# Kernel optimization log

Measured on AMD Instinct MI355X. Metric: run time of the kernel, lower is better.

## Reference

```python
import jax, jax.numpy as jnp
import numpy as np

B, T, NU, NX = 64, 512, 256, 1024


def setup_inputs() -> dict:
    key = jax.random.key(0)
    ks = jax.random.split(key, 10)
    s = 1.0 / NX  # default uniform_(-1/units, 1/units) init
    w = lambda k, shape: jax.random.uniform(k, shape, jnp.float32, -s, s)
    return {
        "u": jax.random.normal(ks[0], (B, T, NU), jnp.float32),
        "x0": 0.5 * jax.random.normal(ks[1], (B, NX), jnp.float32),
        "Wz": w(ks[2], (NU, NX)), "Uz": w(ks[3], (NX, NX)), "bz": jnp.zeros((NX,), jnp.float32),
        "Wf": w(ks[4], (NU, NX)), "Uf": w(ks[5], (NX, NX)), "bf": jnp.zeros((NX,), jnp.float32),
        "Wr": w(ks[6], (NU, NX)), "Ur": w(ks[7], (NX, NX)), "br": jnp.zeros((NX,), jnp.float32),
    }


def reference(u, x0, Wz, Uz, bz, Wf, Uf, bf, Wr, Ur, br):
    # Precompute input projections for all timesteps (same math, hoisted out of the scan).
    az = jnp.einsum("btu,un->btn", u, Wz) + bz  # (B,T,NX)
    af = jnp.einsum("btu,un->btn", u, Wf) + bf
    ar = jnp.einsum("btu,un->btn", u, Wr) + br
    # time-major for scan
    az, af, ar = (jnp.transpose(a, (1, 0, 2)) for a in (az, af, ar))

    def step(x, inp):
        iz, if_, ir = inp
        z = jax.nn.sigmoid(iz + x @ Uz)            # update gate
        f = jax.nn.sigmoid(if_ + x @ Uf)           # forget gate
        r = jnp.tanh(ir + (f * x) @ Ur)            # squashed candidate
        x_next = z * x + (1.0 - z) * r
        # io_delay=True: output is the state x(k) at the current instant
        return x_next, x

    _, ys = jax.lax.scan(step, x0, (az, af, ar))   # ys: (T,B,NX)
    return jnp.transpose(ys, (1, 0, 2))            # (B,T,NX)
```

## Files before the change

### kernel.cpp

```cpp
#include <hip/hip_runtime.h>
#include <stdint.h>

#define Bsz  64
#define Tsz  512
#define NUsz 256
#define NXsz 1024

#define NGRP 8
#define GWG  32
#define MB   8
#define NC   32

#define SPIN_MAX (1u << 18)

typedef __attribute__((ext_vector_type(8))) short  short8;
typedef __attribute__((ext_vector_type(4))) float  float4v;
typedef unsigned long long ull;

#define FLAGX_OFF   0
#define FLAGFX_OFF  2048
#define XBUF_OFF    4096
#define XBUF_PG     32768
#define FXBUF_OFF   (XBUF_OFF + NGRP * XBUF_PG)

__device__ __forceinline__ short f2bf(float f) {
  unsigned x = __float_as_uint(f);
  return (short)((x + 0x7fffu + ((x >> 16) & 1u)) >> 16);
}

__global__ void gru_init(const float* __restrict__ x0, unsigned char* __restrict__ ws) {
  unsigned idx = blockIdx.x * 256u + threadIdx.x;
  if (idx < 256u)      ((unsigned*)(ws + FLAGX_OFF))[idx] = 1u;
  else if (idx < 512u) ((unsigned*)(ws + FLAGFX_OFF))[idx - 256u] = 0u;
  unsigned g = idx >> 13, c = (idx >> 8) & 31u, b = (idx >> 5) & 7u, cc = idx & 31u;
  float v = x0[(g * MB + b) * NXsz + c * 32u + cc];
  *(short*)(ws + XBUF_OFF + g * XBUF_PG + c * 512u + b * 64u + cc * 2u) = f2bf(v);
}

__device__ __forceinline__ void wait_flags(const unsigned* f, int lane, unsigned need,
                                           unsigned* dead) {
  if (*dead) return;
  const unsigned* p = f + (lane & 31);
  unsigned spins = 0;
  while (true) {
    unsigned v = __hip_atomic_load(p, __ATOMIC_RELAXED, __HIP_MEMORY_SCOPE_AGENT);
    if (__all((int)(v >= need))) break;
    if (++spins > SPIN_MAX) { *dead = 1u; break; }
    __builtin_amdgcn_s_sleep(1);
  }
  __builtin_amdgcn_fence(__ATOMIC_ACQUIRE, "workgroup");
}

__device__ __forceinline__ short8 ldfragB(const float* __restrict__ U, int col, int k0) {
  short8 s;
  #pragma unroll
  for (int e = 0; e < 8; ++e) s[e] = f2bf(U[(long)(k0 + e) * NXsz + col]);
  return s;
}

#define MFMA(a, b, c) __builtin_amdgcn_mfma_f32_16x16x32_bf16((a), (b), (c), 0, 0, 0)

__launch_bounds__(256, 1)
__global__ void gru_persist(const float* __restrict__ u,  const float* __restrict__ x0,
                            const float* __restrict__ Wz, const float* __restrict__ Uz, const float* __restrict__ bz,
                            const float* __restrict__ Wf, const float* __restrict__ Uf, const float* __restrict__ bfp,
                            const float* __restrict__ Wr, const float* __restrict__ Ur, const float* __restrict__ br,
                            float* __restrict__ out, unsigned char* __restrict__ ws)
{
  __shared__ short zfU[2][32][1000];
  __shared__ float part[4][2][8][33];
  __shared__ float xs[8][33];
  __shared__ float bz_s[32], bf_s[32], br_s[32];

  const int bx   = blockIdx.x;
  const int g    = bx & 7;
  const int rank = bx >> 3;
  const int col0 = rank * NC;
  const int tid  = threadIdx.x;
  const int wv   = tid >> 6;
  const int lane = tid & 63;
  const int q    = lane >> 4;
  const int cl   = lane & 15;

  for (int idx = tid; idx < 2 * 32 * 992; idx += 256) {
    int gate = (idx >= 32 * 992);
    int rem  = idx - gate * (32 * 992);
    int k = rem >> 5, n = rem & 31;
    const float* U = gate ? Uf : Uz;
    zfU[gate][n][k] = f2bf(U[(long)k * NXsz + col0 + n]);
  }
  { int b = tid >> 5, n = tid & 31;
    xs[b][n] = x0[(g * MB + b) * NXsz + col0 + n]; }
  if (tid < 32) {
    bz_s[tid] = bz[col0 + tid];
    bf_s[tid] = bfp[col0 + tid];
    br_s[tid] = br[col0 + tid];
  }

  const int bc0 = col0 + cl;
  short8 rU[16], rW[4], zW[4], fW[4], zU31[2], fU31[2];
  #pragma unroll
  for (int i = 0; i < 8; ++i) {
    int k0 = (wv * 8 + i) * 32 + q * 8;
    rU[i*2+0] = ldfragB(Ur, bc0,      k0);
    rU[i*2+1] = ldfragB(Ur, bc0 + 16, k0);
  }
  #pragma unroll
  for (int i = 0; i < 2; ++i) {
    int k0 = (wv * 2 + i) * 32 + q * 8;
    rW[i*2+0] = ldfragB(Wr, bc0, k0);  rW[i*2+1] = ldfragB(Wr, bc0+16, k0);
    zW[i*2+0] = ldfragB(Wz, bc0, k0);  zW[i*2+1] = ldfragB(Wz, bc0+16, k0);
    fW[i*2+0] = ldfragB(Wf, bc0, k0);  fW[i*2+1] = ldfragB(Wf, bc0+16, k0);
  }
  if (wv == 3) {
    zU31[0] = ldfragB(Uz, bc0, 992 + q*8);  zU31[1] = ldfragB(Uz, bc0+16, 992 + q*8);
    fU31[0] = ldfragB(Uf, bc0, 992 + q*8);  fU31[1] = ldfragB(Uf, bc0+16, 992 + q*8);
  } else {
    #pragma unroll
    for (int e = 0; e < 8; ++e) { zU31[0][e]=0; zU31[1][e]=0; fU31[0][e]=0; fU31[1][e]=0; }
  }
  __syncthreads();

  unsigned* flagx  = (unsigned*)(ws + FLAGX_OFF)  + g * GWG;
  unsigned* flagfx = (unsigned*)(ws + FLAGFX_OFF) + g * GWG;
  unsigned char* xb_base  = ws + XBUF_OFF  + (unsigned)g * XBUF_PG;
  unsigned char* fxb_base = ws + FXBUF_OFF + (unsigned)g * XBUF_PG;

  const int b8 = cl & 7;
  const unsigned arow = (unsigned)(b8 * 64 + q * 16);
  const float* u_row = u + (long)(g * MB + b8) * (Tsz * (long)NUsz);

  const int cb  = lane >> 3;
  const int cc0 = (lane & 7) * 4;

  float zreg[4] = {0.f, 0.f, 0.f, 0.f};
  unsigned dead = 0;

  for (int t = 0; t < Tsz; ++t) {
    const unsigned char* xb  = xb_base  + (t & 1) * 16384;
    unsigned char*       fxb = fxb_base + (t & 1) * 16384;

    if (wv == 2) {
      float4v o = { xs[cb][cc0], xs[cb][cc0+1], xs[cb][cc0+2], xs[cb][cc0+3] };
      *(float4v*)(out + (long)(g*MB+cb) * (Tsz*(long)NXsz) + (long)t*NXsz + col0 + cc0) = o;
    }

    short8 au[2];
    #pragma unroll
    for (int i = 0; i < 2; ++i) {
      const float* up = u_row + (long)t * NUsz + (wv*2 + i) * 32 + q * 8;
      float4v a0 = *(const float4v*)up;
      float4v a1 = *(const float4v*)(up + 4);
      short8 s;
      s[0]=f2bf(a0[0]); s[1]=f2bf(a0[1]); s[2]=f2bf(a0[2]); s[3]=f2bf(a0[3]);
      s[4]=f2bf(a1[0]); s[5]=f2bf(a1[1]); s[6]=f2bf(a1[2]); s[7]=f2bf(a1[3]);
      au[i] = s;
    }
    float4v az0 = {0,0,0,0}, az1 = {0,0,0,0}, af0 = {0,0,0,0}, af1 = {0,0,0,0};
    #pragma unroll
    for (int i = 0; i < 2; ++i) {
      az0 = MFMA(au[i], zW[i*2+0], az0);
      az1 = MFMA(au[i], zW[i*2+1], az1);
      af0 = MFMA(au[i], fW[i*2+0], af0);
      af1 = MFMA(au[i], fW[i*2+1], af1);
    }

    wait_flags(flagx, lane, (unsigned)(t + 1), &dead);
    {
      ull ax[16];
      #pragma unroll
      for (int i = 0; i < 8; ++i) {
        const ull* pp = (const ull*)(xb + arow + (unsigned)((wv*8 + i) * 512));
        ax[2*i]   = __hip_atomic_load(pp,     __ATOMIC_RELAXED, __HIP_MEMORY_SCOPE_AGENT);
        ax[2*i+1] = __hip_atomic_load(pp + 1, __ATOMIC_RELAXED, __HIP_MEMORY_SCOPE_AGENT);
      }
      #pragma unroll
      for (int i = 0; i < 8; ++i) {
        union { ull u2[2]; short8 s8; } cv;
        cv.u2[0] = ax[2*i]; cv.u2[1] = ax[2*i+1];
        const int c = wv*8 + i;
        int koff;
        short8 b00, b01, b10, b11;
        if (i == 7) {
          koff = ((wv == 3) ? 0 : c*32) + q*8;
          b00 = *(const short8*)&zfU[0][cl][koff];
          b01 = *(const short8*)&zfU[0][cl+16][koff];
          b10 = *(const short8*)&zfU[1][cl][koff];
          b11 = *(const short8*)&zfU[1][cl+16][koff];
          if (wv == 3) { b00 = zU31[0]; b01 = zU31[1]; b10 = fU31[0]; b11 = fU31[1]; }
        } else {
          koff = c*32 + q*8;
          b00 = *(const short8*)&zfU[0][cl][koff];
          b01 = *(const short8*)&zfU[0][cl+16][koff];
          b10 = *(const short8*)&zfU[1][cl][koff];
          b11 = *(const short8*)&zfU[1][cl+16][koff];
        }
        az0 = MFMA(cv.s8, b00, az0);
        az1 = MFMA(cv.s8, b01, az1);
        af0 = MFMA(cv.s8, b10, af0);
        af1 = MFMA(cv.s8, b11, af1);
      }
    }

    if (q < 2) {
      #pragma unroll
      for (int r = 0; r < 4; ++r) {
        part[wv][0][q*4+r][cl]      = az0[r];
        part[wv][0][q*4+r][cl + 16] = az1[r];
        part[wv][1][q*4+r][cl]      = af0[r];
        part[wv][1][q*4+r][cl + 16] = af1[r];
      }
    }
    __syncthreads();

    if (wv == 0) {
      #pragma unroll
      for (int j = 0; j < 4; ++j) {
        int c = cc0 + j;
        float s = part[0][0][cb][c] + part[1][0][cb][c] + part[2][0][cb][c] + part[3][0][cb][c] + bz_s[c];
        zreg[j] = 1.f / (1.f + __expf(-s));
      }
    } else if (wv == 1) {
      ull pack = 0;
      #pragma unroll
      for (int j = 0; j < 4; ++j) {
        int c = cc0 + j;
        float s = part[0][1][cb][c] + part[1][1][cb][c] + part[2][1][cb][c] + part[3][1][cb][c] + bf_s[c];
        float f = 1.f / (1.f + __expf(-s));
        pack |= (ull)(unsigned short)f2bf(f * xs[cb][c]) << (16 * j);
      }
      __hip_atomic_store((ull*)(fxb + (unsigned)(rank * 512 + lane * 8)), pack,
                         __ATOMIC_RELAXED, __HIP_MEMORY_SCOPE_AGENT);
      __builtin_amdgcn_fence(__ATOMIC_RELEASE, "workgroup");
      if (lane == 0)
        __hip_atomic_store(flagfx + rank, (unsigned)(t + 1),
                           __ATOMIC_RELAXED, __HIP_MEMORY_SCOPE_AGENT);
    }
    __syncthreads();

    float4v ar0 = {0,0,0,0}, ar1 = {0,0,0,0};
    #pragma unroll
    for (int i = 0; i < 2; ++i) {
      ar0 = MFMA(au[i], rW[i*2+0], ar0);
      ar1 = MFMA(au[i], rW[i*2+1], ar1);
    }

    wait_flags(flagfx, lane, (unsigned)(t + 1), &dead);
    {
      ull ax[16];
      #pragma unroll
      for (int i = 0; i < 8; ++i) {
        const ull* pp = (const ull*)(fxb + arow + (unsigned)((wv*8 + i) * 512));
        ax[2*i]   = __hip_atomic_load(pp,     __ATOMIC_RELAXED, __HIP_MEMORY_SCOPE_AGENT);
        ax[2*i+1] = __hip_atomic_load(pp + 1, __ATOMIC_RELAXED, __HIP_MEMORY_SCOPE_AGENT);
      }
      #pragma unroll
      for (int i = 0; i < 8; ++i) {
        union { ull u2[2]; short8 s8; } cv;
        cv.u2[0] = ax[2*i]; cv.u2[1] = ax[2*i+1];
        ar0 = MFMA(cv.s8, rU[i*2+0], ar0);
        ar1 = MFMA(cv.s8, rU[i*2+1], ar1);
      }
    }

    if (q < 2) {
      #pragma unroll
      for (int r = 0; r < 4; ++r) {
        part[wv][0][q*4+r][cl]      = ar0[r];
        part[wv][0][q*4+r][cl + 16] = ar1[r];
      }
    }
    __syncthreads();

    if (wv == 0) {
      unsigned char* xbn = xb_base + ((t + 1) & 1) * 16384;
      ull pack = 0;
      float xnv[4];
      #pragma unroll
      for (int j = 0; j < 4; ++j) {
        int c = cc0 + j;
        float s = part[0][0][cb][c] + part[1][0][cb][c] + part[2][0][cb][c] + part[3][0][cb][c] + br_s[c];
        s = fminf(fmaxf(s, -15.f), 15.f);
        float e  = __expf(2.f * s);
        float rr = (e - 1.f) / (e + 1.f);
        float xn = zreg[j] * xs[cb][c] + (1.f - zreg[j]) * rr;
        xnv[j] = xn;
        pack |= (ull)(unsigned short)f2bf(xn) << (16 * j);
      }
      #pragma unroll
      for (int j = 0; j < 4; ++j) xs[cb][cc0 + j] = xnv[j];
      __hip_atomic_store((ull*)(xbn + (unsigned)(rank * 512 + lane * 8)), pack,
                         __ATOMIC_RELAXED, __HIP_MEMORY_SCOPE_AGENT);
      __builtin_amdgcn_fence(__ATOMIC_RELEASE, "workgroup");
      if (lane == 0)
        __hip_atomic_store(flagx + rank, (unsigned)(t + 2),
                           __ATOMIC_RELAXED, __HIP_MEMORY_SCOPE_AGENT);
    }
    __syncthreads();
  }
}

extern "C" void kernel_launch(void* const* d_in, const int* in_sizes, int n_in,
                              void* d_out, int out_size, void* d_ws, size_t ws_size,
                              hipStream_t stream) {
  (void)in_sizes; (void)n_in; (void)out_size; (void)ws_size;
  const float* u   = (const float*)d_in[0];
  const float* x0  = (const float*)d_in[1];
  const float* Wz  = (const float*)d_in[2];
  const float* Uz  = (const float*)d_in[3];
  const float* bz  = (const float*)d_in[4];
  const float* Wf  = (const float*)d_in[5];
  const float* Uf  = (const float*)d_in[6];
  const float* bfp = (const float*)d_in[7];
  const float* Wr  = (const float*)d_in[8];
  const float* Ur  = (const float*)d_in[9];
  const float* br  = (const float*)d_in[10];
  float* out = (float*)d_out;
  unsigned char* ws = (unsigned char*)d_ws;

  hipLaunchKernelGGL(gru_init, dim3(256), dim3(256), 0, stream, x0, ws);

  void* args[] = { (void*)&u, (void*)&x0, (void*)&Wz, (void*)&Uz, (void*)&bz,
                   (void*)&Wf, (void*)&Uf, (void*)&bfp,
                   (void*)&Wr, (void*)&Ur, (void*)&br, (void*)&out, (void*)&ws };
  hipError_t e = hipLaunchCooperativeKernel((const void*)gru_persist, dim3(256), dim3(256),
                                            args, 0, stream);
  if (e != hipSuccess) {
    hipLaunchKernelGGL(gru_persist, dim3(256), dim3(256), 0, stream,
                       u, x0, Wz, Uz, bz, Wf, Uf, bfp, Wr, Ur, br, out, ws);
  }
}
```

Measured before the change: 3.169 ms.

## Halve persistent grid to 4 groups of 16 batch rows with XCD-aware mapping

Restructures the persistent GRU so each workgroup handles 16 batch rows instead of 8, which uses all 16 MFMA rows rather than discarding half. The grid shrinks to 128 workgroups in 4 groups of 32 column slices, and each group is mapped onto one pair of XCDs so its flag and state traffic stays more local. The exchange buffer layout, publish offsets and init kernel are reworked for the 16-row tiles. This trades half the CU count and more per-workgroup epilogue work for fewer wasted MFMA rows and fewer groups synchronising through memory.

```diff
diff --git a/kernel.cpp b/kernel.cpp
--- a/kernel.cpp
+++ b/kernel.cpp
@@ -6,9 +6,9 @@
 #define NUsz 256
 #define NXsz 1024
 
-#define NGRP 8
+#define NGRP 4
 #define GWG  32
-#define MB   8
+#define MB   16
 #define NC   32
 
 #define SPIN_MAX (1u << 18)
@@ -20,7 +20,7 @@
 #define FLAGX_OFF   0
 #define FLAGFX_OFF  2048
 #define XBUF_OFF    4096
-#define XBUF_PG     32768
+#define XBUF_PG     65536
 #define FXBUF_OFF   (XBUF_OFF + NGRP * XBUF_PG)
 
 __device__ __forceinline__ short f2bf(float f) {
@@ -30,11 +30,14 @@
 
 __global__ void gru_init(const float* __restrict__ x0, unsigned char* __restrict__ ws) {
   unsigned idx = blockIdx.x * 256u + threadIdx.x;
-  if (idx < 256u)      ((unsigned*)(ws + FLAGX_OFF))[idx] = 1u;
-  else if (idx < 512u) ((unsigned*)(ws + FLAGFX_OFF))[idx - 256u] = 0u;
-  unsigned g = idx >> 13, c = (idx >> 8) & 31u, b = (idx >> 5) & 7u, cc = idx & 31u;
-  float v = x0[(g * MB + b) * NXsz + c * 32u + cc];
-  *(short*)(ws + XBUF_OFF + g * XBUF_PG + c * 512u + b * 64u + cc * 2u) = f2bf(v);
+  unsigned* flagx  = (unsigned*)(ws + FLAGX_OFF);
+  unsigned* flagfx = (unsigned*)(ws + FLAGFX_OFF);
+  if (idx < 128u)                       flagx[idx] = 1u;
+  else if (idx >= 256u && idx < 384u)   flagfx[idx - 256u] = 0u;
+  unsigned g = idx >> 14, rem = idx & 16383u;
+  unsigned jj = rem >> 8, b = (rem >> 4) & 15u, k = rem & 15u;
+  float v = x0[(g * 16u + b) * NXsz + jj * 16u + k];
+  *(short*)(ws + XBUF_OFF + g * XBUF_PG + jj * 512u + b * 32u + k * 2u) = f2bf(v);
 }
 
 __device__ __forceinline__ void wait_flags(const unsigned* f, int lane, unsigned need,
@@ -68,19 +71,20 @@
                             float* __restrict__ out, unsigned char* __restrict__ ws)
 {
   __shared__ short zfU[2][32][1000];
-  __shared__ float part[4][2][8][33];
-  __shared__ float xs[8][33];
+  __shared__ float part[4][2][16][33];
+  __shared__ float xs[16][33];
   __shared__ float bz_s[32], bf_s[32], br_s[32];
 
   const int bx   = blockIdx.x;
-  const int g    = bx & 7;
-  const int rank = bx >> 3;
-  const int col0 = rank * NC;
+  const int xcd  = bx & 7;
+  const int g    = xcd >> 1;
+  const int j    = ((xcd & 1) << 4) | (bx >> 3);
   const int tid  = threadIdx.x;
   const int wv   = tid >> 6;
   const int lane = tid & 63;
   const int q    = lane >> 4;
   const int cl   = lane & 15;
+  const int col0 = j * NC;
 
   for (int idx = tid; idx < 2 * 32 * 992; idx += 256) {
     int gate = (idx >= 32 * 992);
@@ -89,8 +93,10 @@
     const float* U = gate ? Uf : Uz;
     zfU[gate][n][k] = f2bf(U[(long)k * NXsz + col0 + n]);
   }
-  { int b = tid >> 5, n = tid & 31;
-    xs[b][n] = x0[(g * MB + b) * NXsz + col0 + n]; }
+  for (int idx = tid; idx < 512; idx += 256) {
+    int b = idx >> 5, n = idx & 31;
+    xs[b][n] = x0[(g * MB + b) * NXsz + col0 + n];
+  }
   if (tid < 32) {
     bz_s[tid] = bz[col0 + tid];
     bf_s[tid] = bfp[col0 + tid];
@@ -123,37 +129,45 @@
 
   unsigned* flagx  = (unsigned*)(ws + FLAGX_OFF)  + g * GWG;
   unsigned* flagfx = (unsigned*)(ws + FLAGFX_OFF) + g * GWG;
-  unsigned char* xb_base  = ws + XBUF_OFF  + (unsigned)g * XBUF_PG;
-  unsigned char* fxb_base = ws + FXBUF_OFF + (unsigned)g * XBUF_PG;
-
-  const int b8 = cl & 7;
-  const unsigned arow = (unsigned)(b8 * 64 + q * 16);
-  const float* u_row = u + (long)(g * MB + b8) * (Tsz * (long)NUsz);
-
-  const int cb  = lane >> 3;
-  const int cc0 = (lane & 7) * 4;
-
-  float zreg[4] = {0.f, 0.f, 0.f, 0.f};
+  unsigned char* xb_base  = ws + XBUF_OFF  + g * XBUF_PG;
+  unsigned char* fxb_base = ws + FXBUF_OFF + g * XBUF_PG;
+
+  const unsigned lane_off = (unsigned)(cl * 32 + (q & 1) * 16 + (q >> 1) * 512);
+
+  const int cb  = lane >> 2;
+  const int cc0 = (lane & 3) << 3;
+  const unsigned pub_off = (unsigned)((2*j + (cc0 >> 4)) * 512 + cb * 32 + (cc0 & 15) * 2);
+
+  const long uTN = (long)Tsz * NUsz;
+  const float* u_row = u + (long)(g * MB + cl) * uTN;
+
+  float zreg[8];
+  #pragma unroll
+  for (int i = 0; i < 8; ++i) zreg[i] = 0.f;
   unsigned dead = 0;
 
   for (int t = 0; t < Tsz; ++t) {
-    const unsigned char* xb  = xb_base  + (t & 1) * 16384;
-    unsigned char*       fxb = fxb_base + (t & 1) * 16384;
+    const int p = t & 1;
+    const unsigned char* xb  = xb_base  + p * 32768;
+    unsigned char*       fxb = fxb_base + p * 32768;
 
     if (wv == 2) {
-      float4v o = { xs[cb][cc0], xs[cb][cc0+1], xs[cb][cc0+2], xs[cb][cc0+3] };
-      *(float4v*)(out + (long)(g*MB+cb) * (Tsz*(long)NXsz) + (long)t*NXsz + col0 + cc0) = o;
+      float* op = out + (long)(g * MB + cb) * ((long)Tsz * NXsz) + (long)t * NXsz + col0 + cc0;
+      float4v o0 = { xs[cb][cc0],   xs[cb][cc0+1], xs[cb][cc0+2], xs[cb][cc0+3] };
+      float4v o1 = { xs[cb][cc0+4], xs[cb][cc0+5], xs[cb][cc0+6], xs[cb][cc0+7] };
+      *(float4v*)op = o0;
+      *(float4v*)(op + 4) = o1;
     }
 
     short8 au[2];
     #pragma unroll
     for (int i = 0; i < 2; ++i) {
-      const float* up = u_row + (long)t * NUsz + (wv*2 + i) * 32 + q * 8;
-      float4v a0 = *(const float4v*)up;
-      float4v a1 = *(const float4v*)(up + 4);
+      const float* up = u_row + (long)t * NUsz + (wv * 2 + i) * 32 + q * 8;
+      float4v u0 = *(const float4v*)up;
+      float4v u1 = *(const float4v*)(up + 4);
       short8 s;
-      s[0]=f2bf(a0[0]); s[1]=f2bf(a0[1]); s[2]=f2bf(a0[2]); s[3]=f2bf(a0[3]);
-      s[4]=f2bf(a1[0]); s[5]=f2bf(a1[1]); s[6]=f2bf(a1[2]); s[7]=f2bf(a1[3]);
+      s[0]=f2bf(u0[0]); s[1]=f2bf(u0[1]); s[2]=f2bf(u0[2]); s[3]=f2bf(u0[3]);
+      s[4]=f2bf(u1[0]); s[5]=f2bf(u1[1]); s[6]=f2bf(u1[2]); s[7]=f2bf(u1[3]);
       au[i] = s;
     }
     float4v az0 = {0,0,0,0}, az1 = {0,0,0,0}, af0 = {0,0,0,0}, af1 = {0,0,0,0};
@@ -170,7 +184,7 @@
       ull ax[16];
       #pragma unroll
       for (int i = 0; i < 8; ++i) {
-        const ull* pp = (const ull*)(xb + arow + (unsigned)((wv*8 + i) * 512));
+        const ull* pp = (const ull*)(xb + lane_off + (unsigned)((wv * 8 + i) * 1024));
         ax[2*i]   = __hip_atomic_load(pp,     __ATOMIC_RELAXED, __HIP_MEMORY_SCOPE_AGENT);
         ax[2*i+1] = __hip_atomic_load(pp + 1, __ATOMIC_RELAXED, __HIP_MEMORY_SCOPE_AGENT);
       }
@@ -178,18 +192,17 @@
       for (int i = 0; i < 8; ++i) {
         union { ull u2[2]; short8 s8; } cv;
         cv.u2[0] = ax[2*i]; cv.u2[1] = ax[2*i+1];
-        const int c = wv*8 + i;
-        int koff;
+        const int c = wv * 8 + i;
         short8 b00, b01, b10, b11;
         if (i == 7) {
-          koff = ((wv == 3) ? 0 : c*32) + q*8;
+          int koff = ((wv == 3) ? 0 : c*32) + q*8;
           b00 = *(const short8*)&zfU[0][cl][koff];
           b01 = *(const short8*)&zfU[0][cl+16][koff];
           b10 = *(const short8*)&zfU[1][cl][koff];
           b11 = *(const short8*)&zfU[1][cl+16][koff];
           if (wv == 3) { b00 = zU31[0]; b01 = zU31[1]; b10 = fU31[0]; b11 = fU31[1]; }
         } else {
-          koff = c*32 + q*8;
+          int koff = c*32 + q*8;
           b00 = *(const short8*)&zfU[0][cl][koff];
           b01 = *(const short8*)&zfU[0][cl+16][koff];
           b10 = *(const short8*)&zfU[1][cl][koff];
@@ -201,40 +214,39 @@
         af1 = MFMA(cv.s8, b11, af1);
       }
     }
-
-    if (q < 2) {
-      #pragma unroll
-      for (int r = 0; r < 4; ++r) {
-        part[wv][0][q*4+r][cl]      = az0[r];
-        part[wv][0][q*4+r][cl + 16] = az1[r];
-        part[wv][1][q*4+r][cl]      = af0[r];
-        part[wv][1][q*4+r][cl + 16] = af1[r];
-      }
+    #pragma unroll
+    for (int r = 0; r < 4; ++r) {
+      part[wv][0][q*4+r][cl]      = az0[r];
+      part[wv][0][q*4+r][cl + 16] = az1[r];
+      part[wv][1][q*4+r][cl]      = af0[r];
+      part[wv][1][q*4+r][cl + 16] = af1[r];
     }
     __syncthreads();
 
     if (wv == 0) {
       #pragma unroll
-      for (int j = 0; j < 4; ++j) {
-        int c = cc0 + j;
+      for (int jj2 = 0; jj2 < 8; ++jj2) {
+        int c = cc0 + jj2;
         float s = part[0][0][cb][c] + part[1][0][cb][c] + part[2][0][cb][c] + part[3][0][cb][c] + bz_s[c];
-        zreg[j] = 1.f / (1.f + __expf(-s));
+        zreg[jj2] = 1.f / (1.f + __expf(-s));
       }
     } else if (wv == 1) {
-      ull pack = 0;
-      #pragma unroll
-      for (int j = 0; j < 4; ++j) {
-        int c = cc0 + j;
+      ull pk0 = 0, pk1 = 0;
+      #pragma unroll
+      for (int jj2 = 0; jj2 < 8; ++jj2) {
+        int c = cc0 + jj2;
         float s = part[0][1][cb][c] + part[1][1][cb][c] + part[2][1][cb][c] + part[3][1][cb][c] + bf_s[c];
         float f = 1.f / (1.f + __expf(-s));
-        pack |= (ull)(unsigned short)f2bf(f * xs[cb][c]) << (16 * j);
-      }
-      __hip_atomic_store((ull*)(fxb + (unsigned)(rank * 512 + lane * 8)), pack,
-                         __ATOMIC_RELAXED, __HIP_MEMORY_SCOPE_AGENT);
+        ull h = (ull)(unsigned short)f2bf(f * xs[cb][c]);
+        if (jj2 < 4) pk0 |= h << (16 * jj2);
+        else         pk1 |= h << (16 * (jj2 - 4));
+      }
+      ull* dp = (ull*)(fxb + pub_off);
+      __hip_atomic_store(dp,     pk0, __ATOMIC_RELAXED, __HIP_MEMORY_SCOPE_AGENT);
+      __hip_atomic_store(dp + 1, pk1, __ATOMIC_RELAXED, __HIP_MEMORY_SCOPE_AGENT);
       __builtin_amdgcn_fence(__ATOMIC_RELEASE, "workgroup");
       if (lane == 0)
-        __hip_atomic_store(flagfx + rank, (unsigned)(t + 1),
-                           __ATOMIC_RELAXED, __HIP_MEMORY_SCOPE_AGENT);
+        __hip_atomic_store(flagfx + j, (unsigned)(t + 1), __ATOMIC_RELAXED, __HIP_MEMORY_SCOPE_AGENT);
     }
     __syncthreads();
 
@@ -244,13 +256,12 @@
       ar0 = MFMA(au[i], rW[i*2+0], ar0);
       ar1 = MFMA(au[i], rW[i*2+1], ar1);
     }
-
     wait_flags(flagfx, lane, (unsigned)(t + 1), &dead);
     {
       ull ax[16];
       #pragma unroll
       for (int i = 0; i < 8; ++i) {
-        const ull* pp = (const ull*)(fxb + arow + (unsigned)((wv*8 + i) * 512));
+        const ull* pp = (const ull*)(fxb + lane_off + (unsigned)((wv * 8 + i) * 1024));
         ax[2*i]   = __hip_atomic_load(pp,     __ATOMIC_RELAXED, __HIP_MEMORY_SCOPE_AGENT);
         ax[2*i+1] = __hip_atomic_load(pp + 1, __ATOMIC_RELAXED, __HIP_MEMORY_SCOPE_AGENT);
       }
@@ -262,39 +273,38 @@
         ar1 = MFMA(cv.s8, rU[i*2+1], ar1);
       }
     }
-
-    if (q < 2) {
-      #pragma unroll
-      for (int r = 0; r < 4; ++r) {
-        part[wv][0][q*4+r][cl]      = ar0[r];
-        part[wv][0][q*4+r][cl + 16] = ar1[r];
-      }
+    #pragma unroll
+    for (int r = 0; r < 4; ++r) {
+      part[wv][0][q*4+r][cl]      = ar0[r];
+      part[wv][0][q*4+r][cl + 16] = ar1[r];
     }
     __syncthreads();
 
     if (wv == 0) {
-      unsigned char* xbn = xb_base + ((t + 1) & 1) * 16384;
-      ull pack = 0;
-      float xnv[4];
-      #pragma unroll
-      for (int j = 0; j < 4; ++j) {
-        int c = cc0 + j;
+      unsigned char* xbn = xb_base + ((t + 1) & 1) * 32768;
+      ull pk0 = 0, pk1 = 0;
+      float xnv[8];
+      #pragma unroll
+      for (int jj2 = 0; jj2 < 8; ++jj2) {
+        int c = cc0 + jj2;
         float s = part[0][0][cb][c] + part[1][0][cb][c] + part[2][0][cb][c] + part[3][0][cb][c] + br_s[c];
         s = fminf(fmaxf(s, -15.f), 15.f);
         float e  = __expf(2.f * s);
         float rr = (e - 1.f) / (e + 1.f);
-        float xn = zreg[j] * xs[cb][c] + (1.f - zreg[j]) * rr;
-        xnv[j] = xn;
-        pack |= (ull)(unsigned short)f2bf(xn) << (16 * j);
-      }
-      #pragma unroll
-      for (int j = 0; j < 4; ++j) xs[cb][cc0 + j] = xnv[j];
-      __hip_atomic_store((ull*)(xbn + (unsigned)(rank * 512 + lane * 8)), pack,
-                         __ATOMIC_RELAXED, __HIP_MEMORY_SCOPE_AGENT);
+        float xn = zreg[jj2] * xs[cb][c] + (1.f - zreg[jj2]) * rr;
+        xnv[jj2] = xn;
+        ull h = (ull)(unsigned short)f2bf(xn);
+        if (jj2 < 4) pk0 |= h << (16 * jj2);
+        else         pk1 |= h << (16 * (jj2 - 4));
+      }
+      ull* dp = (ull*)(xbn + pub_off);
+      __hip_atomic_store(dp,     pk0, __ATOMIC_RELAXED, __HIP_MEMORY_SCOPE_AGENT);
+      __hip_atomic_store(dp + 1, pk1, __ATOMIC_RELAXED, __HIP_MEMORY_SCOPE_AGENT);
+      #pragma unroll
+      for (int jj2 = 0; jj2 < 8; ++jj2) xs[cb][cc0 + jj2] = xnv[jj2];
       __builtin_amdgcn_fence(__ATOMIC_RELEASE, "workgroup");
       if (lane == 0)
-        __hip_atomic_store(flagx + rank, (unsigned)(t + 2),
-                           __ATOMIC_RELAXED, __HIP_MEMORY_SCOPE_AGENT);
+        __hip_atomic_store(flagx + j, (unsigned)(t + 2), __ATOMIC_RELAXED, __HIP_MEMORY_SCOPE_AGENT);
     }
     __syncthreads();
   }
@@ -323,10 +333,10 @@
   void* args[] = { (void*)&u, (void*)&x0, (void*)&Wz, (void*)&Uz, (void*)&bz,
                    (void*)&Wf, (void*)&Uf, (void*)&bfp,
                    (void*)&Wr, (void*)&Ur, (void*)&br, (void*)&out, (void*)&ws };
-  hipError_t e = hipLaunchCooperativeKernel((const void*)gru_persist, dim3(256), dim3(256),
+  hipError_t e = hipLaunchCooperativeKernel((const void*)gru_persist, dim3(128), dim3(256),
                                             args, 0, stream);
   if (e != hipSuccess) {
-    hipLaunchKernelGGL(gru_persist, dim3(256), dim3(256), 0, stream,
+    hipLaunchKernelGGL(gru_persist, dim3(128), dim3(256), 0, stream,
                        u, x0, Wz, Uz, bz, Wf, Uf, bfp, Wr, Ur, br, out, ws);
   }
 }
```

Measured after the change: 3.192 ms. Within noise of the previous version (+0.7%).
